# Performance work log

Hardware: AMD Instinct MI355X
Metric: run time of the kernel (lower is better)

The kernel has to match this reference:

```python
import jax, jax.numpy as jnp
import numpy as np

B, S, HIDDEN, H, HD = 4, 1024, 1024, 16, 64  # head_dim = hidden/heads; rel-pos 'd_model' = HD
TABLE = 2 * HD - 1  # 127


def setup_inputs() -> dict:
    key = jax.random.key(0)
    ks = jax.random.split(key, 16)
    sc = 0.02
    return {
        "query": jax.random.normal(ks[0], (B, S, HIDDEN), jnp.float32),
        "key": jax.random.normal(ks[1], (B, S, HIDDEN), jnp.float32),
        "value": jax.random.normal(ks[2], (B, S, HIDDEN), jnp.float32),
        "Wq": jax.random.normal(ks[3], (H, HIDDEN, HD), jnp.float32) * sc,
        "Wk": jax.random.normal(ks[4], (H, HIDDEN, HD), jnp.float32) * sc,
        "Wv": jax.random.normal(ks[5], (H, HIDDEN, HD), jnp.float32) * sc,
        "bq": jax.random.normal(ks[6], (H, HD), jnp.float32) * sc,
        "bk": jax.random.normal(ks[7], (H, HD), jnp.float32) * sc,
        "bv": jax.random.normal(ks[8], (H, HD), jnp.float32) * sc,
        "rp_k_table": jax.random.normal(ks[9], (TABLE, HD), jnp.float32) * sc,
        "rp_v_table": jax.random.normal(ks[10], (TABLE, HD), jnp.float32) * sc,
        "Wfc": jax.random.normal(ks[11], (HIDDEN, HIDDEN), jnp.float32) * sc,
        "bfc": jax.random.normal(ks[12], (HIDDEN,), jnp.float32) * sc,
    }


def _rel_bias(table, length, hd):
    # distance clipped to [-(hd-1), hd-1], shifted -> index into (2*hd-1, hd) table
    i = jnp.arange(length)
    idx = jnp.clip(i[None, :] - i[:, None], -(hd - 1), hd - 1) + (hd - 1)
    return table[idx]  # [S, S, hd]


def reference(query, key, value, Wq, Wk, Wv, bq, bk, bv, rp_k_table, rp_v_table, Wfc, bfc):
    hd = Wq.shape[-1]
    b, s, _ = query.shape
    k_bias = _rel_bias(rp_k_table, s, hd)  # [S,S,hd], shared across heads
    v_bias = _rel_bias(rp_v_table, s, hd)
    # per-head projections: [B,H,S,hd]
    q = jnp.einsum('bsh,nhd->bnsd', query, Wq) + bq[None, :, None, :]
    kk = jnp.einsum('bsh,nhd->bnsd', key, Wk) + bk[None, :, None, :]
    v = jnp.einsum('bsh,nhd->bnsd', value, Wv) + bv[None, :, None, :]
    # scores: QK^T plus Shaw-style relative-position key bias
    scores = (jnp.einsum('bnid,bnjd->bnij', q, kk)
              + jnp.einsum('bnid,ijd->bnij', q, k_bias)) / (hd ** 0.5)
    w = jax.nn.softmax(scores, axis=-1)  # [B,H,S,S]
    out = (jnp.einsum('bnij,bnjd->bnid', w, v)
           + jnp.einsum('bnij,ijd->bnid', w, v_bias))  # [B,H,S,hd]
    hidden = out.transpose(0, 2, 1, 3).reshape(b, s, -1)  # concat heads
    return hidden @ Wfc.T + bfc
```

## Files before the change

### kernel.cpp

```cpp
#include <hip/hip_runtime.h>
#include <stdint.h>

typedef unsigned int u32;
typedef unsigned short u16;
typedef float f32x4 __attribute__((ext_vector_type(4)));
typedef __bf16 bfx8 __attribute__((ext_vector_type(8)));
typedef short s16x8 __attribute__((ext_vector_type(8)));
typedef short s16x4 __attribute__((ext_vector_type(4)));
typedef int i32x4 __attribute__((ext_vector_type(4)));

#define DEVI static __device__ __forceinline__

#if __has_builtin(__builtin_amdgcn_exp2f)
#define EXP2(x) __builtin_amdgcn_exp2f(x)
#else
#define EXP2(x) exp2f(x)
#endif


DEVI u16 f2bf(float f){
  u32 u = __builtin_bit_cast(u32, f);
  u32 r = (u + 0x7fffu + ((u >> 16) & 1u)) >> 16;
  return (u16)r;
}
DEVI float b2f(u16 v){ return __builtin_bit_cast(float, (u32)v << 16); }
DEVI short e2s(float f){ return __builtin_bit_cast(short, (__bf16)f); }

struct s16x4p { s16x4 lo, hi; };
DEVI s16x8 cat4(s16x4 lo, s16x4 hi){ s16x4p p{lo, hi}; return __builtin_bit_cast(s16x8, p); }

DEVI f32x4 mfma16(s16x8 a, s16x8 b, f32x4 c){
  return __builtin_amdgcn_mfma_f32_16x16x32_bf16(
      __builtin_bit_cast(bfx8, a), __builtin_bit_cast(bfx8, b), c, 0, 0, 0);
}

DEVI void gld16(const void* g, void* l){
  __builtin_amdgcn_global_load_lds(
      (__attribute__((address_space(1))) void*)g,
      (__attribute__((address_space(3))) void*)l, 16, 0, 0);
}

__global__ void cast3_kernel(const float* __restrict__ a, const float* __restrict__ b,
                             const float* __restrict__ c, u16* __restrict__ dst){
  const long n_each = 4194304;
  long stride = (long)gridDim.x * blockDim.x;
  for (long v = (long)blockIdx.x * blockDim.x + threadIdx.x; v < 3 * n_each / 8; v += stride){
    long idx8 = v * 8;
    int which = (int)(idx8 / n_each);
    long off = idx8 - (long)which * n_each;
    const float* s = which == 0 ? a : (which == 1 ? b : c);
    float4 f0 = *(const float4*)(s + off);
    float4 f1 = *(const float4*)(s + off + 4);
    s16x8 o;
    o[0]=(short)f2bf(f0.x); o[1]=(short)f2bf(f0.y); o[2]=(short)f2bf(f0.z); o[3]=(short)f2bf(f0.w);
    o[4]=(short)f2bf(f1.x); o[5]=(short)f2bf(f1.y); o[6]=(short)f2bf(f1.z); o[7]=(short)f2bf(f1.w);
    *(s16x8*)(dst + idx8) = o;
  }
}

__global__ void cast1_kernel(const float* __restrict__ a, u16* __restrict__ dst, long n){
  long stride = (long)gridDim.x * blockDim.x;
  for (long v = (long)blockIdx.x * blockDim.x + threadIdx.x; v < n / 8; v += stride){
    long idx8 = v * 8;
    float4 f0 = *(const float4*)(a + idx8);
    float4 f1 = *(const float4*)(a + idx8 + 4);
    s16x8 o;
    o[0]=(short)f2bf(f0.x); o[1]=(short)f2bf(f0.y); o[2]=(short)f2bf(f0.z); o[3]=(short)f2bf(f0.w);
    o[4]=(short)f2bf(f1.x); o[5]=(short)f2bf(f1.y); o[6]=(short)f2bf(f1.z); o[7]=(short)f2bf(f1.w);
    *(s16x8*)(dst + idx8) = o;
  }
}

__global__ void wtrans_kernel(const float* __restrict__ Wq, const float* __restrict__ Wk,
                              const float* __restrict__ Wv, u16* __restrict__ Wt){
  int bid = blockIdx.x;
  int kt = bid & 15; int h = (bid >> 4) & 15; int proj = bid >> 8;
  const float* W = (proj == 0 ? Wq : (proj == 1 ? Wk : Wv)) + (long)h * (1024 * 64);
  __shared__ u16 lt[64][66];
  int t = threadIdx.x;
  #pragma unroll
  for (int it = 0; it < 16; ++it){
    int idx = it * 256 + t;
    int r = idx >> 6, d = idx & 63;
    lt[r][d] = f2bf(W[(long)(kt * 64 + r) * 64 + d]);
  }
  __syncthreads();
  long outbase = (long)proj * 1024 + h * 64;
  #pragma unroll
  for (int it = 0; it < 16; ++it){
    int idx = it * 256 + t;
    int d = idx >> 6, r = idx & 63;
    Wt[(outbase + d) * 1024 + kt * 64 + r] = lt[r][d];
  }
}

__global__ void tables_kernel(const float* __restrict__ rpk, const float* __restrict__ rpv,
                              u16* __restrict__ rpkb, u16* __restrict__ rpvT){
  int t = threadIdx.x;
  for (int i = t; i < 128 * 64; i += 256){
    int row = i >> 6, d = i & 63;
    rpkb[i] = (row < 127) ? f2bf(rpk[row * 64 + d]) : (u16)0;
  }
  for (int i = t; i < 64 * 128; i += 256){
    int d = i >> 7, row = i & 127;
    rpvT[i] = (row < 127) ? f2bf(rpv[row * 64 + d]) : (u16)0;
  }
}

__global__ void vtrans_kernel(const u16* __restrict__ Vb, u16* __restrict__ Vt){
  int bid = blockIdx.x;
  int st = bid & 15, bh = bid >> 4;
  const u16* src = Vb + ((long)bh * 1024 + st * 64) * 64;
  u16* dst = Vt + (long)bh * 64 * 1024 + st * 64;
  __shared__ u16 lt[64][66];
  int t = threadIdx.x;
  #pragma unroll
  for (int it = 0; it < 16; ++it){
    int idx = it * 256 + t;
    int r = idx >> 6, d = idx & 63;
    lt[r][d] = src[idx];
  }
  __syncthreads();
  #pragma unroll
  for (int it = 0; it < 16; ++it){
    int idx = it * 256 + t;
    int d = idx >> 6, r = idx & 63;
    dst[(long)d * 1024 + r] = lt[r][d];
  }
}

DEVI void gemm_core(const u16* __restrict__ A, const u16* __restrict__ Bt,
                    int m0, int n0, u16* lds, int tid, f32x4 (&acc)[4][4]){
  const int K = 1024;
  int w = tid >> 6, lane = tid & 63, g = lane >> 4, li = lane & 15;
  int wm = w >> 1, wn = w & 1;
  for (int ks = 0; ks < 16; ++ks){
    int k0 = ks * 64;
    __syncthreads();
    #pragma unroll
    for (int i = 0; i < 4; ++i){
      int c = i * 256 + w * 64 + lane;
      int r = c >> 3, s = lane & 7;
      int kk = k0 + ((s ^ (r & 7)) << 3);
      gld16(A + (long)(m0 + r) * K + kk, (char*)lds + (i * 256 + w * 64) * 16);
      gld16(Bt + (long)(n0 + r) * K + kk, (char*)lds + 16384 + (i * 256 + w * 64) * 16);
    }
    __syncthreads();
    #pragma unroll
    for (int kh = 0; kh < 2; ++kh){
      s16x8 af[4], bfr[4];
      #pragma unroll
      for (int mi = 0; mi < 4; ++mi){
        int row = wm * 64 + mi * 16 + li;
        int byt = (row * 128 + (kh * 32 + g * 8) * 2) ^ ((li & 7) << 4);
        af[mi] = *(const s16x8*)((const char*)lds + byt);
      }
      #pragma unroll
      for (int ni = 0; ni < 4; ++ni){
        int row = wn * 64 + ni * 16 + li;
        int byt = 16384 + ((row * 128 + (kh * 32 + g * 8) * 2) ^ ((li & 7) << 4));
        bfr[ni] = *(const s16x8*)((const char*)lds + byt);
      }
      #pragma unroll
      for (int mi = 0; mi < 4; ++mi)
        #pragma unroll
        for (int ni = 0; ni < 4; ++ni)
          acc[mi][ni] = mfma16(af[mi], bfr[ni], acc[mi][ni]);
    }
  }
}

__launch_bounds__(256, 2)
__global__ void gemm_qkv(const u16* __restrict__ Xb, const u16* __restrict__ Wt,
                         const float* __restrict__ bq, const float* __restrict__ bk,
                         const float* __restrict__ bv,
                         u16* __restrict__ Qb, u16* __restrict__ Kb, u16* __restrict__ Vb){
  __shared__ __align__(16) u16 lds[16384];
  int tid = threadIdx.x;
  int bo = blockIdx.x;
  int bidx = (bo & 7) * 96 + (bo >> 3);
  int bn = bidx % 24, bm = bidx / 24;
  int m0 = bm * 128, n0 = bn * 128;
  int proj = n0 >> 10;
  const u16* A = Xb + (long)proj * 4096 * 1024;
  f32x4 acc[4][4] = {};
  gemm_core(A, Wt, m0, n0, lds, tid, acc);
  int w = tid >> 6, lane = tid & 63, g = lane >> 4, li = lane & 15;
  int wm = w >> 1, wn = w & 1;
  const float* bias = proj == 0 ? bq : (proj == 1 ? bk : bv);
  u16* Dst = proj == 0 ? Qb : (proj == 1 ? Kb : Vb);
  float scale = (proj == 0) ? 0.125f * 1.44269504f : 1.0f;
  #pragma unroll
  for (int mi = 0; mi < 4; ++mi)
    #pragma unroll
    for (int ni = 0; ni < 4; ++ni)
      #pragma unroll
      for (int r = 0; r < 4; ++r){
        int m = m0 + wm * 64 + mi * 16 + g * 4 + r;
        int n = n0 + wn * 64 + ni * 16 + li;
        int nn = n & 1023;
        float v = (acc[mi][ni][r] + bias[nn]) * scale;
        int b = m >> 10, s = m & 1023;
        int h = nn >> 6, d = nn & 63;
        Dst[((long)(b * 16 + h) * 1024 + s) * 64 + d] = f2bf(v);
      }
}

__launch_bounds__(256, 2)
__global__ void gemm_fc(const u16* __restrict__ Hid, const u16* __restrict__ Wfcb,
                        const float* __restrict__ bfc, float* __restrict__ out){
  __shared__ __align__(16) u16 lds[16384];
  int tid = threadIdx.x;
  int bidx = blockIdx.x;
  int bn = bidx & 7, bm = bidx >> 3;
  int m0 = bm * 128, n0 = bn * 128;
  f32x4 acc[4][4] = {};
  gemm_core(Hid, Wfcb, m0, n0, lds, tid, acc);
  int w = tid >> 6, lane = tid & 63, g = lane >> 4, li = lane & 15;
  int wm = w >> 1, wn = w & 1;
  #pragma unroll
  for (int mi = 0; mi < 4; ++mi)
    #pragma unroll
    for (int ni = 0; ni < 4; ++ni)
      #pragma unroll
      for (int r = 0; r < 4; ++r){
        int m = m0 + wm * 64 + mi * 16 + g * 4 + r;
        int n = n0 + wn * 64 + ni * 16 + li;
        out[(long)m * 1024 + n] = acc[mi][ni][r] + bfc[n];
      }
}

__launch_bounds__(256, 2)
__global__ void attn_kernel(const u16* __restrict__ Qb, const u16* __restrict__ Kb,
                            const u16* __restrict__ Vt, const u16* __restrict__ rpkb,
                            const u16* __restrict__ rpvT, u16* __restrict__ Hid){
  const int S = 1024;
  int bh = blockIdx.y;
  int i0 = blockIdx.x * 64;
  int bb = bh >> 4, hh = bh & 15;
  const u16* Qp = Qb + (long)bh * S * 64;
  const u16* Kp = Kb + (long)bh * S * 64;
  const u16* Vp = Vt + (long)bh * 64 * S;
  int tid = threadIdx.x, w = tid >> 6, lane = tid & 63, g = lane >> 4, li = lane & 15;

  __shared__ __align__(16) char smem[35840];
  u16* rqb  = (u16*)smem;
  u16* bw   = (u16*)(smem + 16384);
  float* redL = (float*)(smem + 32768);
  float* redR = redL + 256;
  float* redD = redR + 256;
  float* Ored = (float*)smem;

  s16x8 qf[4][2];
  #pragma unroll
  for (int ni = 0; ni < 4; ++ni)
    #pragma unroll
    for (int kh = 0; kh < 2; ++kh)
      qf[ni][kh] = *(const s16x8*)(Qp + (long)(i0 + ni * 16 + li) * 64 + kh * 32 + g * 8);

  {
    i32x4 z = {0, 0, 0, 0};
    #pragma unroll
    for (int i = 0; i < 4; ++i) ((i32x4*)bw)[i * 256 + tid] = z;
  }

  #pragma unroll
  for (int tt = 0; tt < 2; ++tt){
    int tb = w * 2 + tt;
    s16x8 pf0 = *(const s16x8*)(rpkb + (tb * 16 + li) * 64 + g * 8);
    s16x8 pf1 = *(const s16x8*)(rpkb + (tb * 16 + li) * 64 + 32 + g * 8);
    #pragma unroll
    for (int ni = 0; ni < 4; ++ni){
      f32x4 r = {0.f, 0.f, 0.f, 0.f};
      r = mfma16(qf[ni][0], pf0, r);
      r = mfma16(qf[ni][1], pf1, r);
      #pragma unroll
      for (int e = 0; e < 4; ++e)
        rqb[(ni * 16 + g * 4 + e) * 128 + tb * 16 + li] = f2bf(r[e]);
    }
  }
  __syncthreads();

  float rqL[4], rqR[4];
  #pragma unroll
  for (int ni = 0; ni < 4; ++ni){
    int iloc = ni * 16 + li;
    rqL[ni] = b2f(rqb[iloc * 128]);
    rqR[ni] = b2f(rqb[iloc * 128 + 126]);
  }

  f32x4 oacc[4][4] = {};
  float dacc[4] = {0, 0, 0, 0}, Lac[4] = {0, 0, 0, 0}, Rac[4] = {0, 0, 0, 0};

  auto LOADKV = [&](int jt, s16x8 (&kf)[2][2], s16x8 (&vv)[4]){
    int jw = jt * 128 + w * 32;
    #pragma unroll
    for (int mi = 0; mi < 2; ++mi)
      #pragma unroll
      for (int kh = 0; kh < 2; ++kh)
        kf[mi][kh] = *(const s16x8*)(Kp + (long)(jw + mi * 16 + li) * 64 + kh * 32 + g * 8);
    #pragma unroll
    for (int nd = 0; nd < 4; ++nd){
      const u16* vp = Vp + (long)(nd * 16 + li) * S + jw + g * 4;
      s16x4 vlo = *(const s16x4*)(vp);
      s16x4 vhi = *(const s16x4*)(vp + 16);
      vv[nd] = cat4(vlo, vhi);
    }
  };

  auto BODY = [&](int jt, s16x8 (&kf)[2][2], s16x8 (&vv)[4],
                  s16x8 (&kfn)[2][2], s16x8 (&vvn)[4]){
    LOADKV(jt + 1, kfn, vvn);
    int jw = jt * 128 + w * 32;
    s16x8 av[4];
    #pragma unroll
    for (int mi = 0; mi < 2; ++mi){
      int js0 = jw + mi * 16;
      f32x4 sacc[4];
      #pragma unroll
      for (int ni = 0; ni < 4; ++ni){
        f32x4 s0 = {0.f, 0.f, 0.f, 0.f};
        s0 = mfma16(kf[mi][0], qf[ni][0], s0);
        s0 = mfma16(kf[mi][1], qf[ni][1], s0);
        sacc[ni] = s0;
      }
      if (js0 >= i0 + 126){
        #pragma unroll
        for (int ni = 0; ni < 4; ++ni)
          #pragma unroll
          for (int r = 0; r < 4; ++r){
            float e = EXP2(sacc[ni][r] + rqR[ni]);
            Rac[ni] += e;
            av[ni][mi * 4 + r] = e2s(e);
          }
      } else if (js0 + 78 <= i0){
        #pragma unroll
        for (int ni = 0; ni < 4; ++ni)
          #pragma unroll
          for (int r = 0; r < 4; ++r){
            float e = EXP2(sacc[ni][r] + rqL[ni]);
            Lac[ni] += e;
            av[ni][mi * 4 + r] = e2s(e);
          }
      } else {
        #pragma unroll
        for (int ni = 0; ni < 4; ++ni){
          int iloc = ni * 16 + li;
          #pragma unroll
          for (int r = 0; r < 4; ++r){
            int jgl = js0 + g * 4 + r;
            int delta = jgl - (i0 + iloc);
            int dcl = delta < -62 ? -62 : (delta > 62 ? 62 : delta);
            int tg = dcl + 63;
            float rqv = b2f(rqb[iloc * 128 + tg]);
            bool lft = delta < -62, rgt = delta > 62;
            rqv = lft ? rqL[ni] : (rgt ? rqR[ni] : rqv);
            float e = EXP2(sacc[ni][r] + rqv);
            short eb = e2s(e);
            av[ni][mi * 4 + r] = eb;
            if (!lft && !rgt){
              int byt = (iloc * 256 + tg * 2) ^ ((iloc & 7) << 4);
              *(u16*)((char*)bw + byt) = (u16)eb;
              dacc[ni] += e;
            }
            Lac[ni] += lft ? e : 0.f;
            Rac[ni] += rgt ? e : 0.f;
          }
        }
      }
    }
    #pragma unroll
    for (int nd = 0; nd < 4; ++nd)
      #pragma unroll
      for (int ni = 0; ni < 4; ++ni)
        oacc[ni][nd] = mfma16(av[ni], vv[nd], oacc[ni][nd]);
  };

  s16x8 kfA[2][2], kfB[2][2], vvA[4], vvB[4];
  LOADKV(0, kfA, vvA);
  for (int jtp = 0; jtp < 4; ++jtp){
    BODY(2 * jtp,     kfA, vvA, kfB, vvB);
    BODY(2 * jtp + 1, kfB, vvB, kfA, vvA);
  }

  #pragma unroll
  for (int ni = 0; ni < 4; ++ni){
    dacc[ni] += __shfl_xor(dacc[ni], 16); dacc[ni] += __shfl_xor(dacc[ni], 32);
    Lac[ni]  += __shfl_xor(Lac[ni], 16);  Lac[ni]  += __shfl_xor(Lac[ni], 32);
    Rac[ni]  += __shfl_xor(Rac[ni], 16);  Rac[ni]  += __shfl_xor(Rac[ni], 32);
  }
  if (g == 0){
    #pragma unroll
    for (int ni = 0; ni < 4; ++ni){
      redL[w * 64 + ni * 16 + li] = Lac[ni];
      redR[w * 64 + ni * 16 + li] = Rac[ni];
      redD[w * 64 + ni * 16 + li] = dacc[ni];
    }
  }
  __syncthreads();
  if (tid < 64){
    int i = tid;
    float Ls = redL[i] + redL[64 + i] + redL[128 + i] + redL[192 + i];
    float Rs = redR[i] + redR[64 + i] + redR[128 + i] + redR[192 + i];
    float Ds = redD[i] + redD[64 + i] + redD[128 + i] + redD[192 + i] + Ls + Rs;
    *(u16*)((char*)bw + ((i * 256 + 0)   ^ ((i & 7) << 4))) = f2bf(Ls);
    *(u16*)((char*)bw + ((i * 256 + 252) ^ ((i & 7) << 4))) = f2bf(Rs);
    redD[i] = Ds;
  }
  for (int ww = 0; ww < 4; ++ww){
    if (w == ww){
      #pragma unroll
      for (int ni = 0; ni < 4; ++ni)
        #pragma unroll
        for (int nd = 0; nd < 4; ++nd)
          #pragma unroll
          for (int r = 0; r < 4; ++r){
            int i = ni * 16 + g * 4 + r, d = nd * 16 + li;
            if (ww == 0) Ored[i * 64 + d] = oacc[ni][nd][r];
            else         Ored[i * 64 + d] += oacc[ni][nd][r];
          }
    }
    __syncthreads();
  }
  s16x8 rvf[4];
  #pragma unroll
  for (int ksl = 0; ksl < 4; ++ksl)
    rvf[ksl] = *(const s16x8*)(rpvT + (w * 16 + li) * 128 + ksl * 32 + g * 8);
  f32x4 bacc[4];
  #pragma unroll
  for (int mi = 0; mi < 4; ++mi){
    f32x4 a4 = {0.f, 0.f, 0.f, 0.f};
    #pragma unroll
    for (int ksl = 0; ksl < 4; ++ksl){
      int row = mi * 16 + li;
      int byt = (row * 256 + (ksl * 32 + g * 8) * 2) ^ ((row & 7) << 4);
      s16x8 a = *(const s16x8*)((const char*)bw + byt);
      a4 = mfma16(a, rvf[ksl], a4);
    }
    bacc[mi] = a4;
  }
  #pragma unroll
  for (int mi = 0; mi < 4; ++mi)
    #pragma unroll
    for (int r = 0; r < 4; ++r){
      int i = mi * 16 + g * 4 + r;
      float den = redD[i];
      float o = (Ored[i * 64 + w * 16 + li] + bacc[mi][r]) / den;
      Hid[((long)bb * S + i0 + i) * 1024 + hh * 64 + w * 16 + li] = f2bf(o);
    }
}

extern "C" void kernel_launch(void* const* d_in, const int* in_sizes, int n_in,
                              void* d_out, int out_size, void* d_ws, size_t ws_size,
                              hipStream_t stream){
  const float* query = (const float*)d_in[0];
  const float* key   = (const float*)d_in[1];
  const float* value = (const float*)d_in[2];
  const float* Wq  = (const float*)d_in[3];
  const float* Wk  = (const float*)d_in[4];
  const float* Wv  = (const float*)d_in[5];
  const float* bq  = (const float*)d_in[6];
  const float* bk  = (const float*)d_in[7];
  const float* bv  = (const float*)d_in[8];
  const float* rpk = (const float*)d_in[9];
  const float* rpv = (const float*)d_in[10];
  const float* Wfc = (const float*)d_in[11];
  const float* bfc = (const float*)d_in[12];
  float* out = (float*)d_out;

  u16* Xb   = (u16*)d_ws;
  u16* Wt   = Xb + 3L * 4096 * 1024;
  u16* Wfcb = Wt + 3072L * 1024;
  u16* rpkb = Wfcb + 1024L * 1024;
  u16* rpvT = rpkb + 128 * 64;
  u16* Qb   = rpvT + 64 * 128;
  u16* Kb   = Qb + 64L * 1024 * 64;
  u16* Vb   = Kb + 64L * 1024 * 64;
  u16* Vt   = Vb + 64L * 1024 * 64;
  u16* Hid  = Vt + 64L * 1024 * 64;

  cast3_kernel<<<2048, 256, 0, stream>>>(query, key, value, Xb);
  cast1_kernel<<<512, 256, 0, stream>>>(Wfc, Wfcb, 1024L * 1024);
  wtrans_kernel<<<768, 256, 0, stream>>>(Wq, Wk, Wv, Wt);
  tables_kernel<<<1, 256, 0, stream>>>(rpk, rpv, rpkb, rpvT);
  gemm_qkv<<<768, 256, 0, stream>>>(Xb, Wt, bq, bk, bv, Qb, Kb, Vb);
  vtrans_kernel<<<1024, 256, 0, stream>>>(Vb, Vt);
  attn_kernel<<<dim3(16, 64), 256, 0, stream>>>(Qb, Kb, Vt, rpkb, rpvT, Hid);
  gemm_fc<<<256, 256, 0, stream>>>(Hid, Wfcb, bfc, out);
}
```

Baseline: 263.9 us.

## Stage K and V tiles cooperatively through swizzled shared memory in attention

Replaces per-wave direct global loads of K/V fragments (with register double-buffering) by block-cooperative 16-byte global-to-LDS copies of each 128-key tile into XOR-swizzled shared buffers, then reads MFMA fragments from LDS. Intends to make global loads fully coalesced, especially for the transposed V rows. Adds two barriers per tile, removes the register prefetch overlap, and nearly doubles shared memory use, which may limit occupancy.

```diff
diff --git a/kernel.cpp b/kernel.cpp
--- a/kernel.cpp
+++ b/kernel.cpp
@@ -243,13 +243,15 @@
   const u16* Vp = Vt + (long)bh * 64 * S;
   int tid = threadIdx.x, w = tid >> 6, lane = tid & 63, g = lane >> 4, li = lane & 15;
 
-  __shared__ __align__(16) char smem[35840];
-  u16* rqb  = (u16*)smem;
-  u16* bw   = (u16*)(smem + 16384);
-  float* redL = (float*)(smem + 32768);
+  __shared__ __align__(16) char smem[65536];
+  u16* klds = (u16*)smem;
+  u16* vlds = (u16*)(smem + 16384);
+  u16* rqb  = (u16*)(smem + 32768);
+  u16* bwb  = (u16*)(smem + 49152);
+  float* redL = (float*)smem;
   float* redR = redL + 256;
   float* redD = redR + 256;
-  float* Ored = (float*)smem;
+  float* Ored = (float*)rqb;
 
   s16x8 qf[4][2];
   #pragma unroll
@@ -261,7 +263,7 @@
   {
     i32x4 z = {0, 0, 0, 0};
     #pragma unroll
-    for (int i = 0; i < 4; ++i) ((i32x4*)bw)[i * 256 + tid] = z;
+    for (int i = 0; i < 4; ++i) ((i32x4*)bwb)[i * 256 + tid] = z;
   }
 
   #pragma unroll
@@ -292,30 +294,49 @@
   f32x4 oacc[4][4] = {};
   float dacc[4] = {0, 0, 0, 0}, Lac[4] = {0, 0, 0, 0}, Rac[4] = {0, 0, 0, 0};
 
-  auto LOADKV = [&](int jt, s16x8 (&kf)[2][2], s16x8 (&vv)[4]){
-    int jw = jt * 128 + w * 32;
-    #pragma unroll
-    for (int mi = 0; mi < 2; ++mi)
-      #pragma unroll
-      for (int kh = 0; kh < 2; ++kh)
-        kf[mi][kh] = *(const s16x8*)(Kp + (long)(jw + mi * 16 + li) * 64 + kh * 32 + g * 8);
+  for (int jt = 0; jt < 8; ++jt){
+    int jb = jt * 128;
+    __syncthreads();
+    #pragma unroll
+    for (int p2 = 0; p2 < 4; ++p2){
+      int idx = p2 * 256 + tid;
+      int r = idx >> 3, s8 = idx & 7;
+      int kk = (s8 ^ (r & 7)) << 3;
+      gld16(Kp + (long)(jb + r) * 64 + kk, (char*)klds + idx * 16);
+    }
+    #pragma unroll
+    for (int p2 = 0; p2 < 4; ++p2){
+      int idx = p2 * 256 + tid;
+      int d = idx >> 4, c16 = idx & 15;
+      int cb = (c16 * 16) ^ ((d & 15) << 4);
+      gld16(Vp + (long)d * S + jb + (cb >> 1), (char*)vlds + idx * 16);
+    }
+    __syncthreads();
+
+    int jw = w * 32;
+    s16x8 kf[2][2];
+    #pragma unroll
+    for (int p = 0; p < 2; ++p)
+      #pragma unroll
+      for (int kh = 0; kh < 2; ++kh){
+        int row = jw + p * 16 + li;
+        int byt = (row * 128 + (kh * 32 + g * 8) * 2) ^ ((li & 7) << 4);
+        kf[p][kh] = *(const s16x8*)((const char*)klds + byt);
+      }
+    s16x8 vv[4];
     #pragma unroll
     for (int nd = 0; nd < 4; ++nd){
-      const u16* vp = Vp + (long)(nd * 16 + li) * S + jw + g * 4;
-      s16x4 vlo = *(const s16x4*)(vp);
-      s16x4 vhi = *(const s16x4*)(vp + 16);
+      int d = nd * 16 + li;
+      int o1 = (jw * 2 + g * 8) ^ ((li & 15) << 4);
+      int o2 = (jw * 2 + g * 8 + 32) ^ ((li & 15) << 4);
+      s16x4 vlo = *(const s16x4*)((const char*)vlds + d * 256 + o1);
+      s16x4 vhi = *(const s16x4*)((const char*)vlds + d * 256 + o2);
       vv[nd] = cat4(vlo, vhi);
     }
-  };
-
-  auto BODY = [&](int jt, s16x8 (&kf)[2][2], s16x8 (&vv)[4],
-                  s16x8 (&kfn)[2][2], s16x8 (&vvn)[4]){
-    LOADKV(jt + 1, kfn, vvn);
-    int jw = jt * 128 + w * 32;
     s16x8 av[4];
     #pragma unroll
     for (int mi = 0; mi < 2; ++mi){
-      int js0 = jw + mi * 16;
+      int js0 = jb + jw + mi * 16;
       f32x4 sacc[4];
       #pragma unroll
       for (int ni = 0; ni < 4; ++ni){
@@ -360,7 +381,7 @@
             av[ni][mi * 4 + r] = eb;
             if (!lft && !rgt){
               int byt = (iloc * 256 + tg * 2) ^ ((iloc & 7) << 4);
-              *(u16*)((char*)bw + byt) = (u16)eb;
+              *(u16*)((char*)bwb + byt) = (u16)eb;
               dacc[ni] += e;
             }
             Lac[ni] += lft ? e : 0.f;
@@ -374,15 +395,9 @@
       #pragma unroll
       for (int ni = 0; ni < 4; ++ni)
         oacc[ni][nd] = mfma16(av[ni], vv[nd], oacc[ni][nd]);
-  };
-
-  s16x8 kfA[2][2], kfB[2][2], vvA[4], vvB[4];
-  LOADKV(0, kfA, vvA);
-  for (int jtp = 0; jtp < 4; ++jtp){
-    BODY(2 * jtp,     kfA, vvA, kfB, vvB);
-    BODY(2 * jtp + 1, kfB, vvB, kfA, vvA);
-  }
-
+  }
+
+  __syncthreads();
   #pragma unroll
   for (int ni = 0; ni < 4; ++ni){
     dacc[ni] += __shfl_xor(dacc[ni], 16); dacc[ni] += __shfl_xor(dacc[ni], 32);
@@ -403,8 +418,8 @@
     float Ls = redL[i] + redL[64 + i] + redL[128 + i] + redL[192 + i];
     float Rs = redR[i] + redR[64 + i] + redR[128 + i] + redR[192 + i];
     float Ds = redD[i] + redD[64 + i] + redD[128 + i] + redD[192 + i] + Ls + Rs;
-    *(u16*)((char*)bw + ((i * 256 + 0)   ^ ((i & 7) << 4))) = f2bf(Ls);
-    *(u16*)((char*)bw + ((i * 256 + 252) ^ ((i & 7) << 4))) = f2bf(Rs);
+    *(u16*)((char*)bwb + ((i * 256 + 0)   ^ ((i & 7) << 4))) = f2bf(Ls);
+    *(u16*)((char*)bwb + ((i * 256 + 252) ^ ((i & 7) << 4))) = f2bf(Rs);
     redD[i] = Ds;
   }
   for (int ww = 0; ww < 4; ++ww){
@@ -434,7 +449,7 @@
     for (int ksl = 0; ksl < 4; ++ksl){
       int row = mi * 16 + li;
       int byt = (row * 256 + (ksl * 32 + g * 8) * 2) ^ ((row & 7) << 4);
-      s16x8 a = *(const s16x8*)((const char*)bw + byt);
+      s16x8 a = *(const s16x8*)((const char*)bwb + byt);
       a4 = mfma16(a, rvf[ksl], a4);
     }
     bacc[mi] = a4;
```

Result: faster. 258.3 us (-2.1%).
